# Performance work log

Hardware: AMD Instinct MI355X
Metric: run time of the kernel (lower is better)

## Reference

```python
import jax, jax.numpy as jnp
import numpy as np

B, NV, NDIRS, NRINGS, C, NF = 2, 30000, 8, 3, 16, 16


def setup_inputs() -> dict:
    key = jax.random.key(0)
    k1, k2, k3, k4, k5 = jax.random.split(key, 5)
    y = jax.random.normal(k1, (B, NV, NDIRS, C), dtype=jnp.float32)
    # sync_field: for each (batch, vertex, ring, dir) an index triple (b, v, d) into y
    v_idx = jax.random.randint(k2, (B, NV, NRINGS, NDIRS), 0, NV)
    d_idx = jax.random.randint(k3, (B, NV, NRINGS, NDIRS), 0, NDIRS)
    b_idx = jnp.broadcast_to(jnp.arange(B)[:, None, None, None], (B, NV, NRINGS, NDIRS))
    sync_field = jnp.stack([b_idx, v_idx, d_idx], axis=-1).astype(jnp.int32)
    kernel = jax.random.normal(k4, (NRINGS, NDIRS, C, NF), dtype=jnp.float32) * 0.05
    center_kernel = jax.random.normal(k5, (C, NF), dtype=jnp.float32) * 0.05
    bias = jnp.zeros((NF,), dtype=jnp.float32)
    return {"y": y, "sync_field": sync_field, "kernel": kernel,
            "center_kernel": center_kernel, "bias": bias}


def reference(y, sync_field, kernel, center_kernel, bias):
    b, nv, ndirs, c = y.shape
    nrings = kernel.shape[0]
    nf = kernel.shape[-1]
    # tf.gather_nd: index triples (batch, vertex, dir) -> channel vectors
    patches = y[sync_field[..., 0], sync_field[..., 1], sync_field[..., 2]]  # (b, nv, nrings, ndirs, c)
    patches = patches.reshape(b * nv, nrings, ndirs, c)
    # circular padding along direction axis: width becomes 2*ndirs-1
    patches = jnp.concatenate([patches, patches[:, :, :-1, :]], axis=2)
    # valid conv with (nrings, ndirs) kernel -> (b*nv, 1, ndirs, nf)
    out = jax.lax.conv_general_dilated(
        patches, kernel, window_strides=(1, 1), padding='VALID',
        dimension_numbers=('NHWC', 'HWIO', 'NHWC'))
    out = out.reshape(b, nv, ndirs, nf)
    out = out + jnp.einsum('bvdc,cf->bvdf', y, center_kernel) + bias
    out = jax.nn.relu(out)
    return jnp.max(out, axis=2)  # take_max over directions -> (b, nv, nf)
```

## Files before the change

### kernel.cpp

```cpp
#include <hip/hip_runtime.h>

static constexpr int kB = 2;
static constexpr int kNV = 30000;
static constexpr int kD = 8;
static constexpr int kR = 3;
static constexpr int kC = 16;
static constexpr int kF = 16;
static constexpr int NP = (kB * kNV) / 2;
static constexpr int NWAVES = 3840;

typedef short short8  __attribute__((ext_vector_type(8)));
typedef float floatx4 __attribute__((ext_vector_type(4)));

static constexpr int PATCH0   = 0;
static constexpr int PATCH_SZ = 1536;
static constexpr int CENT0    = 3072;
static constexpr int CENT_SZ  = 1024;

__device__ __forceinline__ unsigned bf16rne(float x) {
    unsigned u = __float_as_uint(x);
    return (u + 0x7fffu + ((u >> 16) & 1u)) >> 16;
}


__global__ __launch_bounds__(64) void sgc_kernel(
    const float* __restrict__ y,
    const int*   __restrict__ sync_field,
    const float* __restrict__ kern,
    const float* __restrict__ ck,
    const float* __restrict__ bias,
    float*       __restrict__ out)
{
    __shared__ __align__(16) char smem[PATCH_SZ * 2 + CENT_SZ * 2];

    const int lane = threadIdx.x;
    const int wid  = blockIdx.x;
    const int f    = lane & 15;
    const int q    = lane >> 4;
    const int mvtx = (lane >> 3) & 1;
    const int md   = lane & 7;

    {
        const int zofs = CENT0 + (lane >> 5) * CENT_SZ + ((lane >> 1) & 15) * 64
                         + 32 + (lane & 1) * 16;
        *(uint4*)(smem + zofs) = make_uint4(0u, 0u, 0u, 0u);
    }

    int aOfs[12];
    short8 bfrag[13];
#pragma unroll
    for (int kk = 0; kk < 12; ++kk) {
        const int g   = kk * 4 + q;
        const int dd  = (g * 43) >> 8;
        const int rem = g - dd * 6;
        const int r   = rem >> 1;
        const int ch  = rem & 1;
        const int rot = (md + dd) & 7;
        aOfs[kk] = ((mvtx * 3 + r) * 8 + rot) * 32 + ch * 16;
        const int be = ((r * 8 + dd) * 16 + ch * 8) * 16 + f;
        union { unsigned u[4]; short8 v; } t;
#pragma unroll
        for (int j = 0; j < 4; ++j) {
            const float a = kern[be + (2 * j) * 16];
            const float b = kern[be + (2 * j + 1) * 16];
            t.u[j] = bf16rne(a) | (bf16rne(b) << 16);
        }
        bfrag[kk] = t.v;
    }
    {
        union { unsigned u[4]; short8 v; } t;
        if (q < 2) {
#pragma unroll
            for (int j = 0; j < 4; ++j) {
                const float a = ck[(q * 8 + 2 * j) * 16 + f];
                const float b = ck[(q * 8 + 2 * j + 1) * 16 + f];
                t.u[j] = bf16rne(a) | (bf16rne(b) << 16);
            }
        } else {
            t.u[0] = t.u[1] = t.u[2] = t.u[3] = 0u;
        }
        bfrag[12] = t.v;
    }
    const int cOfs = (mvtx * 8 + md) * 64 + q * 16;
    const float biasv = bias[f];

    const bool isPatch = lane < 48;
    int gvtx, gr, gdir;
    if (isPatch) {
        gvtx = (lane >= 24) ? 1 : 0;
        const int rem = lane - gvtx * 24;
        gr   = rem >> 3;
        gdir = rem & 7;
    } else {
        gvtx = (lane >> 3) & 1;
        gr   = 0;
        gdir = lane & 7;
    }
    const int wofs0  = isPatch ? (PATCH0 + ((gvtx * 3 + gr) * 8 + gdir) * 32)
                               : (CENT0 + (gvtx * 8 + gdir) * 64);
    const int wdelta = isPatch ? PATCH_SZ : CENT_SZ;

    float4 g0, g1, g2, g3;
    int sB0 = 0, sB1 = 0, sB2 = 0;
    int p = wid;
    if (p < NP) {
        int go;
        if (isPatch) {
            const int* s = sync_field + (((2 * p + gvtx) * 3 + gr) * 8 + gdir) * 3;
            const int a0 = s[0], a1 = s[1], a2 = s[2];
            go = ((a0 * kNV + a1) * kD + a2) * kC;
        } else {
            go = ((2 * p + gvtx) * kD + gdir) * kC;
        }
        const float4* yp = reinterpret_cast<const float4*>(y + go);
        g0 = yp[0]; g1 = yp[1]; g2 = yp[2]; g3 = yp[3];
        if (p + NWAVES < NP && isPatch) {
            const int* s = sync_field
                + (((2 * (p + NWAVES) + gvtx) * 3 + gr) * 8 + gdir) * 3;
            sB0 = s[0]; sB1 = s[1]; sB2 = s[2];
        }
    }

    int ib = 0;
    while (p < NP) {
        const int pb = PATCH0 + ib * PATCH_SZ;
        const int cb = CENT0 + ib * CENT_SZ;

        {
            unsigned wu[8];
            const float4 gg[4] = { g0, g1, g2, g3 };
#pragma unroll
            for (int i = 0; i < 4; ++i) {
                wu[2 * i]     = bf16rne(gg[i].x) | (bf16rne(gg[i].y) << 16);
                wu[2 * i + 1] = bf16rne(gg[i].z) | (bf16rne(gg[i].w) << 16);
            }
            const int wofs = wofs0 + ib * wdelta;
            *(uint4*)(smem + wofs)      = make_uint4(wu[0], wu[1], wu[2], wu[3]);
            *(uint4*)(smem + wofs + 16) = make_uint4(wu[4], wu[5], wu[6], wu[7]);
        }

        const int pn = p + NWAVES;
        if (pn < NP) {
            int go;
            if (isPatch) go = ((sB0 * kNV + sB1) * kD + sB2) * kC;
            else         go = ((2 * pn + gvtx) * kD + gdir) * kC;
            const float4* yp = reinterpret_cast<const float4*>(y + go);
            g0 = yp[0]; g1 = yp[1]; g2 = yp[2]; g3 = yp[3];
            const int pnn = pn + NWAVES;
            if (pnn < NP && isPatch) {
                const int* s = sync_field
                    + (((2 * pnn + gvtx) * 3 + gr) * 8 + gdir) * 3;
                sB0 = s[0]; sB1 = s[1]; sB2 = s[2];
            }
        }

        __asm__ __volatile__("" ::: "memory");
        __builtin_amdgcn_s_waitcnt(0xC07F);
        __asm__ __volatile__("" ::: "memory");

        floatx4 acc = { biasv, biasv, biasv, biasv };
#pragma unroll
        for (int kk = 0; kk < 12; ++kk) {
            const short8 af = *(const short8*)(smem + pb + aOfs[kk]);
            acc = __builtin_amdgcn_mfma_f32_16x16x32_bf16(af, bfrag[kk], acc, 0, 0, 0);
        }
        {
            const short8 af = *(const short8*)(smem + cb + cOfs);
            acc = __builtin_amdgcn_mfma_f32_16x16x32_bf16(af, bfrag[12], acc, 0, 0, 0);
        }

        float mx = fmaxf(fmaxf(acc[0], acc[1]), fmaxf(acc[2], acc[3]));
        mx = fmaxf(mx, 0.0f);
        mx = fmaxf(mx, __shfl_xor(mx, 16, 64));
        if (((lane >> 4) & 1) == 0)
            out[(2 * p + (lane >> 5)) * kF + f] = mx;

        p = pn;
        ib ^= 1;
    }
}

extern "C" void kernel_launch(void* const* d_in, const int* in_sizes, int n_in,
                              void* d_out, int out_size, void* d_ws, size_t ws_size,
                              hipStream_t stream) {
    const float* y    = reinterpret_cast<const float*>(d_in[0]);
    const int*   sf   = reinterpret_cast<const int*>(d_in[1]);
    const float* kern = reinterpret_cast<const float*>(d_in[2]);
    const float* ck   = reinterpret_cast<const float*>(d_in[3]);
    const float* bias = reinterpret_cast<const float*>(d_in[4]);
    float* out = reinterpret_cast<float*>(d_out);

    sgc_kernel<<<NWAVES, 64, 0, stream>>>(y, sf, kern, ck, bias, out);
}
```

Baseline: 113.2 us.

## Precompute bf16 copy of y and gather offsets in prep kernel

Adds a prep kernel that converts y to bf16 and turns each sync_field triple into a flat element offset, both written to workspace. The main kernel then gathers 32-byte bf16 rows instead of 64-byte float rows. It feeds the centre term straight from registers instead of through shared memory and prefetches two iterations ahead. It also splits the MFMA chain into two accumulators to shorten the dependency chain. The cost is an extra launch and a full extra pass over y and sync_field each call.

```diff
diff --git a/kernel.cpp b/kernel.cpp
--- a/kernel.cpp
+++ b/kernel.cpp
@@ -7,31 +7,56 @@
 static constexpr int kC = 16;
 static constexpr int kF = 16;
 static constexpr int NP = (kB * kNV) / 2;
-static constexpr int NWAVES = 3840;
+static constexpr int S  = 3840;
+
+static constexpr int NY   = kB * kNV * kD * kC;
+static constexpr int NSF  = kB * kNV * kR * kD;
+static constexpr int YCVT_BLOCKS = NY / (256 * 8);
+static constexpr int OFS_BLOCKS  = NSF / 256;
+
+static constexpr size_t WS_OFFS = 16u * 1024u * 1024u;
 
 typedef short short8  __attribute__((ext_vector_type(8)));
 typedef float floatx4 __attribute__((ext_vector_type(4)));
 
-static constexpr int PATCH0   = 0;
 static constexpr int PATCH_SZ = 1536;
-static constexpr int CENT0    = 3072;
-static constexpr int CENT_SZ  = 1024;
 
 __device__ __forceinline__ unsigned bf16rne(float x) {
     unsigned u = __float_as_uint(x);
     return (u + 0x7fffu + ((u >> 16) & 1u)) >> 16;
 }
 
+__global__ __launch_bounds__(256) void prep_kernel(
+    const float* __restrict__ y, const int* __restrict__ sf,
+    unsigned short* __restrict__ yb, int* __restrict__ offs)
+{
+    const int b = blockIdx.x;
+    if (b < YCVT_BLOCKS) {
+        const int t = b * 256 + threadIdx.x;
+        const float4* src = reinterpret_cast<const float4*>(y) + (size_t)t * 2;
+        const float4 a = src[0], c = src[1];
+        uint4 o;
+        o.x = bf16rne(a.x) | (bf16rne(a.y) << 16);
+        o.y = bf16rne(a.z) | (bf16rne(a.w) << 16);
+        o.z = bf16rne(c.x) | (bf16rne(c.y) << 16);
+        o.w = bf16rne(c.z) | (bf16rne(c.w) << 16);
+        reinterpret_cast<uint4*>(yb)[t] = o;
+    } else {
+        const int t = (b - YCVT_BLOCKS) * 256 + threadIdx.x;
+        const int* s = sf + (size_t)t * 3;
+        offs[t] = ((s[0] * kNV + s[1]) * kD + s[2]) * kC;
+    }
+}
 
 __global__ __launch_bounds__(64) void sgc_kernel(
-    const float* __restrict__ y,
-    const int*   __restrict__ sync_field,
+    const unsigned short* __restrict__ yb,
+    const int*   __restrict__ offs,
     const float* __restrict__ kern,
     const float* __restrict__ ck,
     const float* __restrict__ bias,
     float*       __restrict__ out)
 {
-    __shared__ __align__(16) char smem[PATCH_SZ * 2 + CENT_SZ * 2];
+    __shared__ __align__(16) char smem[2 * PATCH_SZ];
 
     const int lane = threadIdx.x;
     const int wid  = blockIdx.x;
@@ -39,12 +64,6 @@
     const int q    = lane >> 4;
     const int mvtx = (lane >> 3) & 1;
     const int md   = lane & 7;
-
-    {
-        const int zofs = CENT0 + (lane >> 5) * CENT_SZ + ((lane >> 1) & 15) * 64
-                         + 32 + (lane & 1) * 16;
-        *(uint4*)(smem + zofs) = make_uint4(0u, 0u, 0u, 0u);
-    }
 
     int aOfs[12];
     short8 bfrag[13];
@@ -81,102 +100,100 @@
         }
         bfrag[12] = t.v;
     }
-    const int cOfs = (mvtx * 8 + md) * 64 + q * 16;
     const float biasv = bias[f];
 
     const bool isPatch = lane < 48;
-    int gvtx, gr, gdir;
-    if (isPatch) {
-        gvtx = (lane >= 24) ? 1 : 0;
-        const int rem = lane - gvtx * 24;
-        gr   = rem >> 3;
-        gdir = rem & 7;
-    } else {
-        gvtx = (lane >> 3) & 1;
-        gr   = 0;
-        gdir = lane & 7;
-    }
-    const int wofs0  = isPatch ? (PATCH0 + ((gvtx * 3 + gr) * 8 + gdir) * 32)
-                               : (CENT0 + (gvtx * 8 + gdir) * 64);
-    const int wdelta = isPatch ? PATCH_SZ : CENT_SZ;
-
-    float4 g0, g1, g2, g3;
-    int sB0 = 0, sB1 = 0, sB2 = 0;
-    int p = wid;
-    if (p < NP) {
-        int go;
-        if (isPatch) {
-            const int* s = sync_field + (((2 * p + gvtx) * 3 + gr) * 8 + gdir) * 3;
-            const int a0 = s[0], a1 = s[1], a2 = s[2];
-            go = ((a0 * kNV + a1) * kD + a2) * kC;
-        } else {
-            go = ((2 * p + gvtx) * kD + gdir) * kC;
-        }
-        const float4* yp = reinterpret_cast<const float4*>(y + go);
-        g0 = yp[0]; g1 = yp[1]; g2 = yp[2]; g3 = yp[3];
-        if (p + NWAVES < NP && isPatch) {
-            const int* s = sync_field
-                + (((2 * (p + NWAVES) + gvtx) * 3 + gr) * 8 + gdir) * 3;
-            sB0 = s[0]; sB1 = s[1]; sB2 = s[2];
-        }
-    }
-
-    int ib = 0;
+    const int  cRow    = (lane & 15) * 16;
+
+    const int p0 = wid;
+    const int c0 = (p0           < NP) ? p0           : NP - 1;
+    const int c1 = (p0 + S       < NP) ? p0 + S       : NP - 1;
+    const int c2 = (p0 + 2 * S   < NP) ? p0 + 2 * S   : NP - 1;
+
+    uint4 P[2][2];
+    uint4 Cc[2][2];
+    int   off_n = 0;
+    {
+        int o0 = 0, o1 = 0;
+        if (isPatch) {
+            o0 = offs[48 * c0 + lane];
+            o1 = offs[48 * c1 + lane];
+            off_n = offs[48 * c2 + lane];
+        }
+        if (isPatch) {
+            const uint4* gp = reinterpret_cast<const uint4*>(yb + o0);
+            P[0][0] = gp[0]; P[0][1] = gp[1];
+        }
+        {
+            const uint4* gp = reinterpret_cast<const uint4*>(yb + 256 * c0 + cRow);
+            Cc[0][0] = gp[0]; Cc[0][1] = gp[1];
+        }
+        if (isPatch) {
+            const uint4* gp = reinterpret_cast<const uint4*>(yb + o1);
+            P[1][0] = gp[0]; P[1][1] = gp[1];
+        }
+        {
+            const uint4* gp = reinterpret_cast<const uint4*>(yb + 256 * c1 + cRow);
+            Cc[1][0] = gp[0]; Cc[1][1] = gp[1];
+        }
+    }
+
+    int p = p0, cur = 0;
     while (p < NP) {
-        const int pb = PATCH0 + ib * PATCH_SZ;
-        const int cb = CENT0 + ib * CENT_SZ;
-
-        {
-            unsigned wu[8];
-            const float4 gg[4] = { g0, g1, g2, g3 };
-#pragma unroll
-            for (int i = 0; i < 4; ++i) {
-                wu[2 * i]     = bf16rne(gg[i].x) | (bf16rne(gg[i].y) << 16);
-                wu[2 * i + 1] = bf16rne(gg[i].z) | (bf16rne(gg[i].w) << 16);
-            }
-            const int wofs = wofs0 + ib * wdelta;
-            *(uint4*)(smem + wofs)      = make_uint4(wu[0], wu[1], wu[2], wu[3]);
-            *(uint4*)(smem + wofs + 16) = make_uint4(wu[4], wu[5], wu[6], wu[7]);
-        }
-
-        const int pn = p + NWAVES;
-        if (pn < NP) {
-            int go;
-            if (isPatch) go = ((sB0 * kNV + sB1) * kD + sB2) * kC;
-            else         go = ((2 * pn + gvtx) * kD + gdir) * kC;
-            const float4* yp = reinterpret_cast<const float4*>(y + go);
-            g0 = yp[0]; g1 = yp[1]; g2 = yp[2]; g3 = yp[3];
-            const int pnn = pn + NWAVES;
-            if (pnn < NP && isPatch) {
-                const int* s = sync_field
-                    + (((2 * pnn + gvtx) * 3 + gr) * 8 + gdir) * 3;
-                sB0 = s[0]; sB1 = s[1]; sB2 = s[2];
-            }
+        if (isPatch) {
+            char* wp = smem + cur * PATCH_SZ + lane * 32;
+            *(uint4*)(wp)      = P[cur][0];
+            *(uint4*)(wp + 16) = P[cur][1];
+        }
+
+        short8 af12;
+        {
+            union { uint4 u; short8 s; } t0, t1;
+            t0.u = Cc[cur][0]; t1.u = Cc[cur][1];
+            const short8 z8 = { 0, 0, 0, 0, 0, 0, 0, 0 };
+            af12 = (q == 0) ? t0.s : (q == 1) ? t1.s : z8;
         }
 
         __asm__ __volatile__("" ::: "memory");
         __builtin_amdgcn_s_waitcnt(0xC07F);
         __asm__ __volatile__("" ::: "memory");
 
-        floatx4 acc = { biasv, biasv, biasv, biasv };
-#pragma unroll
-        for (int kk = 0; kk < 12; ++kk) {
-            const short8 af = *(const short8*)(smem + pb + aOfs[kk]);
-            acc = __builtin_amdgcn_mfma_f32_16x16x32_bf16(af, bfrag[kk], acc, 0, 0, 0);
-        }
-        {
-            const short8 af = *(const short8*)(smem + cb + cOfs);
-            acc = __builtin_amdgcn_mfma_f32_16x16x32_bf16(af, bfrag[12], acc, 0, 0, 0);
-        }
-
-        float mx = fmaxf(fmaxf(acc[0], acc[1]), fmaxf(acc[2], acc[3]));
+        {
+            const int cn2 = (p + 2 * S < NP) ? p + 2 * S : NP - 1;
+            if (isPatch) {
+                const uint4* gp = reinterpret_cast<const uint4*>(yb + off_n);
+                P[cur][0] = gp[0]; P[cur][1] = gp[1];
+            }
+            {
+                const uint4* gp =
+                    reinterpret_cast<const uint4*>(yb + 256 * cn2 + cRow);
+                Cc[cur][0] = gp[0]; Cc[cur][1] = gp[1];
+            }
+            const int cn3 = (p + 3 * S < NP) ? p + 3 * S : NP - 1;
+            if (isPatch) off_n = offs[48 * cn3 + lane];
+        }
+
+        floatx4 acc0 = { biasv, biasv, biasv, biasv };
+        floatx4 acc1 = { 0.f, 0.f, 0.f, 0.f };
+        const char* pb = smem + cur * PATCH_SZ;
+#pragma unroll
+        for (int kk = 0; kk < 12; kk += 2) {
+            const short8 a0 = *(const short8*)(pb + aOfs[kk]);
+            const short8 a1 = *(const short8*)(pb + aOfs[kk + 1]);
+            acc0 = __builtin_amdgcn_mfma_f32_16x16x32_bf16(a0, bfrag[kk], acc0, 0, 0, 0);
+            acc1 = __builtin_amdgcn_mfma_f32_16x16x32_bf16(a1, bfrag[kk + 1], acc1, 0, 0, 0);
+        }
+        acc0 = __builtin_amdgcn_mfma_f32_16x16x32_bf16(af12, bfrag[12], acc0, 0, 0, 0);
+
+        float mx = fmaxf(fmaxf(acc0[0] + acc1[0], acc0[1] + acc1[1]),
+                         fmaxf(acc0[2] + acc1[2], acc0[3] + acc1[3]));
         mx = fmaxf(mx, 0.0f);
         mx = fmaxf(mx, __shfl_xor(mx, 16, 64));
         if (((lane >> 4) & 1) == 0)
             out[(2 * p + (lane >> 5)) * kF + f] = mx;
 
-        p = pn;
-        ib ^= 1;
+        p += S;
+        cur ^= 1;
     }
 }
 
@@ -190,5 +207,9 @@
     const float* bias = reinterpret_cast<const float*>(d_in[4]);
     float* out = reinterpret_cast<float*>(d_out);
 
-    sgc_kernel<<<NWAVES, 64, 0, stream>>>(y, sf, kern, ck, bias, out);
-}
+    unsigned short* yb = reinterpret_cast<unsigned short*>(d_ws);
+    int* offs = reinterpret_cast<int*>((char*)d_ws + WS_OFFS);
+
+    prep_kernel<<<YCVT_BLOCKS + OFS_BLOCKS, 256, 0, stream>>>(y, sf, yb, offs);
+    sgc_kernel<<<S, 64, 0, stream>>>(yb, offs, kern, ck, bias, out);
+}
```

After: 162.5 us. 1.44x slower.

## Pack four waves per block, feed center MFMA from registers, split accumulators

Applied to the files above, without the earlier changes.

Each block now holds four waves with private LDS double buffers, and the grid is a fixed 7500 waves that each process exactly four vertex pairs in a fully unrolled loop. The center-tap operand is built directly in registers from coalesced y loads instead of being staged through LDS, and the gather uses simple contiguous sync_field indexing. MFMA chains are split into two independent accumulators to shorten the dependency chain. Together these aim to raise occupancy and memory-level parallelism and to cut LDS traffic, at the cost of hardcoding the work split to NP divisible by 7500 and adding one extra vector add per output.

```diff
diff --git a/kernel.cpp b/kernel.cpp
--- a/kernel.cpp
+++ b/kernel.cpp
@@ -7,23 +7,21 @@
 static constexpr int kC = 16;
 static constexpr int kF = 16;
 static constexpr int NP = (kB * kNV) / 2;
-static constexpr int NWAVES = 3840;
+static constexpr int NW = 7500;
+static constexpr int S  = NW;
+static constexpr int WPB = 4;
 
 typedef short short8  __attribute__((ext_vector_type(8)));
 typedef float floatx4 __attribute__((ext_vector_type(4)));
 
-static constexpr int PATCH0   = 0;
 static constexpr int PATCH_SZ = 1536;
-static constexpr int CENT0    = 3072;
-static constexpr int CENT_SZ  = 1024;
 
 __device__ __forceinline__ unsigned bf16rne(float x) {
     unsigned u = __float_as_uint(x);
     return (u + 0x7fffu + ((u >> 16) & 1u)) >> 16;
 }
 
-
-__global__ __launch_bounds__(64) void sgc_kernel(
+__global__ __launch_bounds__(256) void sgc_kernel(
     const float* __restrict__ y,
     const int*   __restrict__ sync_field,
     const float* __restrict__ kern,
@@ -31,20 +29,17 @@
     const float* __restrict__ bias,
     float*       __restrict__ out)
 {
-    __shared__ __align__(16) char smem[PATCH_SZ * 2 + CENT_SZ * 2];
+    __shared__ __align__(16) char smem[WPB * 2 * PATCH_SZ];
 
-    const int lane = threadIdx.x;
-    const int wid  = blockIdx.x;
+    const int lane   = threadIdx.x & 63;
+    const int wlocal = threadIdx.x >> 6;
+    const int wg     = blockIdx.x * WPB + wlocal;
+    char* wbase = smem + wlocal * (2 * PATCH_SZ);
+
     const int f    = lane & 15;
     const int q    = lane >> 4;
     const int mvtx = (lane >> 3) & 1;
     const int md   = lane & 7;
-
-    {
-        const int zofs = CENT0 + (lane >> 5) * CENT_SZ + ((lane >> 1) & 15) * 64
-                         + 32 + (lane & 1) * 16;
-        *(uint4*)(smem + zofs) = make_uint4(0u, 0u, 0u, 0u);
-    }
 
     int aOfs[12];
     short8 bfrag[13];
@@ -81,52 +76,36 @@
         }
         bfrag[12] = t.v;
     }
-    const int cOfs = (mvtx * 8 + md) * 64 + q * 16;
     const float biasv = bias[f];
 
     const bool isPatch = lane < 48;
-    int gvtx, gr, gdir;
-    if (isPatch) {
-        gvtx = (lane >= 24) ? 1 : 0;
-        const int rem = lane - gvtx * 24;
-        gr   = rem >> 3;
-        gdir = rem & 7;
-    } else {
-        gvtx = (lane >> 3) & 1;
-        gr   = 0;
-        gdir = lane & 7;
-    }
-    const int wofs0  = isPatch ? (PATCH0 + ((gvtx * 3 + gr) * 8 + gdir) * 32)
-                               : (CENT0 + (gvtx * 8 + gdir) * 64);
-    const int wdelta = isPatch ? PATCH_SZ : CENT_SZ;
+    const int  cenElem = (lane & 15) * 16;
 
+    int p = wg;
     float4 g0, g1, g2, g3;
+    float4 c0, c1, c2, c3;
     int sB0 = 0, sB1 = 0, sB2 = 0;
-    int p = wid;
-    if (p < NP) {
-        int go;
+    {
         if (isPatch) {
-            const int* s = sync_field + (((2 * p + gvtx) * 3 + gr) * 8 + gdir) * 3;
+            const int* s = sync_field + (size_t)(p * 48 + lane) * 3;
             const int a0 = s[0], a1 = s[1], a2 = s[2];
-            go = ((a0 * kNV + a1) * kD + a2) * kC;
-        } else {
-            go = ((2 * p + gvtx) * kD + gdir) * kC;
+            const float4* gp = reinterpret_cast<const float4*>(
+                y + ((a0 * kNV + a1) * kD + a2) * kC);
+            g0 = gp[0]; g1 = gp[1]; g2 = gp[2]; g3 = gp[3];
         }
-        const float4* yp = reinterpret_cast<const float4*>(y + go);
-        g0 = yp[0]; g1 = yp[1]; g2 = yp[2]; g3 = yp[3];
-        if (p + NWAVES < NP && isPatch) {
-            const int* s = sync_field
-                + (((2 * (p + NWAVES) + gvtx) * 3 + gr) * 8 + gdir) * 3;
+        const float4* cp = reinterpret_cast<const float4*>(y + p * 256 + cenElem);
+        c0 = cp[0]; c1 = cp[1]; c2 = cp[2]; c3 = cp[3];
+        if (isPatch) {
+            const int* s = sync_field + (size_t)((p + S) * 48 + lane) * 3;
             sB0 = s[0]; sB1 = s[1]; sB2 = s[2];
         }
     }
 
-    int ib = 0;
-    while (p < NP) {
-        const int pb = PATCH0 + ib * PATCH_SZ;
-        const int cb = CENT0 + ib * CENT_SZ;
+#pragma unroll
+    for (int it = 0; it < 4; ++it) {
+        char* pb = wbase + (it & 1) * PATCH_SZ;
 
-        {
+        if (isPatch) {
             unsigned wu[8];
             const float4 gg[4] = { g0, g1, g2, g3 };
 #pragma unroll
@@ -134,22 +113,36 @@
                 wu[2 * i]     = bf16rne(gg[i].x) | (bf16rne(gg[i].y) << 16);
                 wu[2 * i + 1] = bf16rne(gg[i].z) | (bf16rne(gg[i].w) << 16);
             }
-            const int wofs = wofs0 + ib * wdelta;
-            *(uint4*)(smem + wofs)      = make_uint4(wu[0], wu[1], wu[2], wu[3]);
-            *(uint4*)(smem + wofs + 16) = make_uint4(wu[4], wu[5], wu[6], wu[7]);
+            char* wp = pb + lane * 32;
+            *(uint4*)(wp)      = make_uint4(wu[0], wu[1], wu[2], wu[3]);
+            *(uint4*)(wp + 16) = make_uint4(wu[4], wu[5], wu[6], wu[7]);
         }
 
-        const int pn = p + NWAVES;
-        if (pn < NP) {
-            int go;
-            if (isPatch) go = ((sB0 * kNV + sB1) * kD + sB2) * kC;
-            else         go = ((2 * pn + gvtx) * kD + gdir) * kC;
-            const float4* yp = reinterpret_cast<const float4*>(y + go);
-            g0 = yp[0]; g1 = yp[1]; g2 = yp[2]; g3 = yp[3];
-            const int pnn = pn + NWAVES;
-            if (pnn < NP && isPatch) {
-                const int* s = sync_field
-                    + (((2 * pnn + gvtx) * 3 + gr) * 8 + gdir) * 3;
+        short8 af12;
+        {
+            const float4 cc[4] = { c0, c1, c2, c3 };
+            const int h = (q < 2) ? q * 2 : 0;
+            union { unsigned u[4]; short8 v; } t;
+            t.u[0] = bf16rne(cc[h].x) | (bf16rne(cc[h].y) << 16);
+            t.u[1] = bf16rne(cc[h].z) | (bf16rne(cc[h].w) << 16);
+            t.u[2] = bf16rne(cc[h + 1].x) | (bf16rne(cc[h + 1].y) << 16);
+            t.u[3] = bf16rne(cc[h + 1].z) | (bf16rne(cc[h + 1].w) << 16);
+            const short8 z8 = { 0, 0, 0, 0, 0, 0, 0, 0 };
+            af12 = (q < 2) ? t.v : z8;
+        }
+
+        if (it < 3) {
+            if (isPatch) {
+                const float4* gp = reinterpret_cast<const float4*>(
+                    y + ((sB0 * kNV + sB1) * kD + sB2) * kC);
+                g0 = gp[0]; g1 = gp[1]; g2 = gp[2]; g3 = gp[3];
+            }
+            const float4* cp =
+                reinterpret_cast<const float4*>(y + (p + S) * 256 + cenElem);
+            c0 = cp[0]; c1 = cp[1]; c2 = cp[2]; c3 = cp[3];
+            if (it < 2 && isPatch) {
+                const int* s =
+                    sync_field + (size_t)((p + 2 * S) * 48 + lane) * 3;
                 sB0 = s[0]; sB1 = s[1]; sB2 = s[2];
             }
         }
@@ -158,25 +151,25 @@
         __builtin_amdgcn_s_waitcnt(0xC07F);
         __asm__ __volatile__("" ::: "memory");
 
-        floatx4 acc = { biasv, biasv, biasv, biasv };
+        floatx4 acc0 = { biasv, biasv, biasv, biasv };
+        floatx4 acc1 = { 0.f, 0.f, 0.f, 0.f };
 #pragma unroll
-        for (int kk = 0; kk < 12; ++kk) {
-            const short8 af = *(const short8*)(smem + pb + aOfs[kk]);
-            acc = __builtin_amdgcn_mfma_f32_16x16x32_bf16(af, bfrag[kk], acc, 0, 0, 0);
+        for (int kk = 0; kk < 12; kk += 2) {
+            const short8 a0 = *(const short8*)(pb + aOfs[kk]);
+            const short8 a1 = *(const short8*)(pb + aOfs[kk + 1]);
+            acc0 = __builtin_amdgcn_mfma_f32_16x16x32_bf16(a0, bfrag[kk], acc0, 0, 0, 0);
+            acc1 = __builtin_amdgcn_mfma_f32_16x16x32_bf16(a1, bfrag[kk + 1], acc1, 0, 0, 0);
         }
-        {
-            const short8 af = *(const short8*)(smem + cb + cOfs);
-            acc = __builtin_amdgcn_mfma_f32_16x16x32_bf16(af, bfrag[12], acc, 0, 0, 0);
-        }
+        acc0 = __builtin_amdgcn_mfma_f32_16x16x32_bf16(af12, bfrag[12], acc0, 0, 0, 0);
 
-        float mx = fmaxf(fmaxf(acc[0], acc[1]), fmaxf(acc[2], acc[3]));
+        float mx = fmaxf(fmaxf(acc0[0] + acc1[0], acc0[1] + acc1[1]),
+                         fmaxf(acc0[2] + acc1[2], acc0[3] + acc1[3]));
         mx = fmaxf(mx, 0.0f);
         mx = fmaxf(mx, __shfl_xor(mx, 16, 64));
         if (((lane >> 4) & 1) == 0)
             out[(2 * p + (lane >> 5)) * kF + f] = mx;
 
-        p = pn;
-        ib ^= 1;
+        p += S;
     }
 }
 
@@ -190,5 +183,5 @@
     const float* bias = reinterpret_cast<const float*>(d_in[4]);
     float* out = reinterpret_cast<float*>(d_out);
 
-    sgc_kernel<<<NWAVES, 64, 0, stream>>>(y, sf, kern, ck, bias, out);
+    sgc_kernel<<<NW / WPB, WPB * 64, 0, stream>>>(y, sf, kern, ck, bias, out);
 }
```

Result: slower. 141.3 us (+24.9%).
